# Performance work log

Hardware: AMD Instinct MI355X
Metric: run time of the kernel (lower is better)

Reference implementation:

```python
import jax, jax.numpy as jnp
import numpy as np

MAXDISP = 48
GROUP = 8
EPS = 1e-5


def setup_inputs() -> dict:
    key = jax.random.key(0)
    k1, k2 = jax.random.split(key)
    x = jax.random.normal(k1, (2, 64, 96, 320), dtype=jnp.float32)
    y = jax.random.normal(k2, (2, 64, 96, 320), dtype=jnp.float32)
    return {"x": x, "y": y}


def reference(x, y):
    # Faithful translation of CostVolume.forward.
    # torch's unfold over left-zero-padded y at kernel position d picks
    # y_pad[..., j + d]; per-window L2 norm over channels reduces to a
    # per-pixel channel norm (padded zeros normalize to zero), so we
    # normalize once and gather shifted columns.
    D = MAXDISP + 1
    b, c, h, w = x.shape
    cpg = c // GROUP
    xg = x.reshape(b, GROUP, cpg, h, w)
    yg = y.reshape(b, GROUP, cpg, h, w)
    xn = xg / (jnp.linalg.norm(xg, axis=2, keepdims=True) + EPS)
    yn = yg / (jnp.linalg.norm(yg, axis=2, keepdims=True) + EPS)
    # left zero-pad width dim by MAXDISP (padded zeros stay zero after norm)
    y_pad = jnp.pad(yn, ((0, 0), (0, 0), (0, 0), (0, 0), (MAXDISP, 0)))
    # after torch.flip on the disparity axis, disparity k compares x[:, j]
    # with y[:, j - k]  ->  padded index j + MAXDISP - k
    idx = jnp.arange(w)[None, :] + MAXDISP - jnp.arange(D)[:, None]  # [D, w]
    y_shift = y_pad[..., idx]  # [b, g, cpg, h, D, w]
    cost = jnp.sum(jnp.abs(xn[:, :, :, :, None, :] - y_shift), axis=2)  # [b,g,h,D,w]
    return jnp.transpose(cost, (0, 1, 3, 2, 4))  # [b, group, D, h, w]
```

## Files before the change

### kernel.cpp

```cpp
#include <hip/hip_runtime.h>


#define MAXDISP 48
#define NDISP   49
#define HH      96
#define WW      320
#define EPSN    1e-5f

__global__ __launch_bounds__(WW) void cost_volume_kernel(
    const float* __restrict__ x, const float* __restrict__ y,
    float* __restrict__ out)
{
    __shared__ float4 ylds[2 * WW];

    const int j   = threadIdx.x;
    const int blk = blockIdx.x;
    const int h   = blk % HH;
    const int bg  = blk / HH;

    const int inBase = bg * 8 * (HH * WW) + h * WW + j;

    float xv[8], yv[8];
    float xs = 0.f, ys = 0.f;
#pragma unroll
    for (int cc = 0; cc < 8; ++cc) {
        float xi = x[inBase + cc * (HH * WW)];
        float yi = y[inBase + cc * (HH * WW)];
        xv[cc] = xi; yv[cc] = yi;
        xs += xi * xi;
        ys += yi * yi;
    }
    const float xinv = 1.f / (sqrtf(xs) + EPSN);
    const float yinv = 1.f / (sqrtf(ys) + EPSN);

    float sAbs = 0.f;
#pragma unroll
    for (int cc = 0; cc < 8; ++cc) {
        xv[cc] *= xinv;
        yv[cc] *= yinv;
        sAbs += fabsf(xv[cc]);
    }

    ylds[j]      = make_float4(yv[0], yv[1], yv[2], yv[3]);
    ylds[WW + j] = make_float4(yv[4], yv[5], yv[6], yv[7]);
    __syncthreads();

    float* outp = out + bg * (NDISP * HH * WW) + h * WW + j;

#pragma unroll 7
    for (int d = 0; d < NDISP; ++d) {
        float cost;
        const int jj = j - d;
        if (jj >= 0) {
            const float4 a = ylds[jj];
            const float4 b = ylds[WW + jj];
            cost = fabsf(xv[0] - a.x) + fabsf(xv[1] - a.y)
                 + fabsf(xv[2] - a.z) + fabsf(xv[3] - a.w)
                 + fabsf(xv[4] - b.x) + fabsf(xv[5] - b.y)
                 + fabsf(xv[6] - b.z) + fabsf(xv[7] - b.w);
        } else {
            cost = sAbs;
        }
        outp[d * (HH * WW)] = cost;
    }
}

extern "C" void kernel_launch(void* const* d_in, const int* in_sizes, int n_in,
                              void* d_out, int out_size, void* d_ws, size_t ws_size,
                              hipStream_t stream) {
    const float* x = (const float*)d_in[0];
    const float* y = (const float*)d_in[1];
    float* out = (float*)d_out;
    dim3 grid(2 * 8 * HH);
    dim3 block(WW);
    cost_volume_kernel<<<grid, block, 0, stream>>>(x, y, out);
}
```

Baseline: 124.4 us.

## Register-tile cost volume over 4 pixels by 4 disparities with float4 stores

Each thread now computes a 4-pixel by 4-disparity tile instead of one pixel across all disparities. The 320 threads are split into 80 pixel quads and 4 disparity chunks. Normalized x and y are kept in LDS in channel-major layout, so y windows can be read with float4 loads and reused across disparities, and outputs are written as float4. This cuts LDS traffic per output and widens the global stores, at the cost of more registers and an uneven disparity split (the first chunk handles 4 groups, the others 3).

```diff
diff --git a/kernel.cpp b/kernel.cpp
--- a/kernel.cpp
+++ b/kernel.cpp
@@ -1,67 +1,108 @@
 #include <hip/hip_runtime.h>
 
 
-#define MAXDISP 48
-#define NDISP   49
-#define HH      96
-#define WW      320
-#define EPSN    1e-5f
+#define HH   96
+#define WW   320
+#define HW   (HH * WW)
+#define NDISP 49
+#define EPSN 1e-5f
 
 __global__ __launch_bounds__(WW) void cost_volume_kernel(
     const float* __restrict__ x, const float* __restrict__ y,
     float* __restrict__ out)
 {
-    __shared__ float4 ylds[2 * WW];
+    __shared__ float xn_s[8][WW];
+    __shared__ float yn_s[8][WW];
 
-    const int j   = threadIdx.x;
+    const int t   = threadIdx.x;
     const int blk = blockIdx.x;
     const int h   = blk % HH;
     const int bg  = blk / HH;
 
-    const int inBase = bg * 8 * (HH * WW) + h * WW + j;
+    const size_t inBase = (size_t)bg * 8 * HW + (size_t)h * WW;
 
-    float xv[8], yv[8];
-    float xs = 0.f, ys = 0.f;
+    {
+        float xv[8], yv[8];
+        float xs = 0.f, ys = 0.f;
+#pragma unroll
+        for (int cc = 0; cc < 8; ++cc) {
+            float xi = x[inBase + (size_t)cc * HW + t];
+            float yi = y[inBase + (size_t)cc * HW + t];
+            xv[cc] = xi; yv[cc] = yi;
+            xs += xi * xi;
+            ys += yi * yi;
+        }
+        const float xinv = 1.f / (sqrtf(xs) + EPSN);
+        const float yinv = 1.f / (sqrtf(ys) + EPSN);
+#pragma unroll
+        for (int cc = 0; cc < 8; ++cc) {
+            xn_s[cc][t] = xv[cc] * xinv;
+            yn_s[cc][t] = yv[cc] * yinv;
+        }
+    }
+    __syncthreads();
+
+    const int q  = t % 80;
+    const int dc = t / 80;
+    const int Q  = q * 4;
+
+    float4 xq[8];
+#pragma unroll
+    for (int cc = 0; cc < 8; ++cc)
+        xq[cc] = *(const float4*)&xn_s[cc][Q];
+
+    float4 sA = make_float4(0.f, 0.f, 0.f, 0.f);
 #pragma unroll
     for (int cc = 0; cc < 8; ++cc) {
-        float xi = x[inBase + cc * (HH * WW)];
-        float yi = y[inBase + cc * (HH * WW)];
-        xv[cc] = xi; yv[cc] = yi;
-        xs += xi * xi;
-        ys += yi * yi;
-    }
-    const float xinv = 1.f / (sqrtf(xs) + EPSN);
-    const float yinv = 1.f / (sqrtf(ys) + EPSN);
-
-    float sAbs = 0.f;
-#pragma unroll
-    for (int cc = 0; cc < 8; ++cc) {
-        xv[cc] *= xinv;
-        yv[cc] *= yinv;
-        sAbs += fabsf(xv[cc]);
+        sA.x += fabsf(xq[cc].x);
+        sA.y += fabsf(xq[cc].y);
+        sA.z += fabsf(xq[cc].z);
+        sA.w += fabsf(xq[cc].w);
     }
 
-    ylds[j]      = make_float4(yv[0], yv[1], yv[2], yv[3]);
-    ylds[WW + j] = make_float4(yv[4], yv[5], yv[6], yv[7]);
-    __syncthreads();
+    const int g0 = (dc == 0) ? 0 : (3 * dc + 1);
+    const int g1 = 3 * dc + 4;
 
-    float* outp = out + bg * (NDISP * HH * WW) + h * WW + j;
+    float* outp = out + (size_t)bg * (NDISP * HW) + (size_t)h * WW + Q;
 
-#pragma unroll 7
-    for (int d = 0; d < NDISP; ++d) {
-        float cost;
-        const int jj = j - d;
-        if (jj >= 0) {
-            const float4 a = ylds[jj];
-            const float4 b = ylds[WW + jj];
-            cost = fabsf(xv[0] - a.x) + fabsf(xv[1] - a.y)
-                 + fabsf(xv[2] - a.z) + fabsf(xv[3] - a.w)
-                 + fabsf(xv[4] - b.x) + fabsf(xv[5] - b.y)
-                 + fabsf(xv[6] - b.z) + fabsf(xv[7] - b.w);
-        } else {
-            cost = sAbs;
+    for (int g = g0; g < g1; ++g) {
+        int wq0 = q - g - 1; if (wq0 < 0) wq0 = 0;
+        int wq1 = q - g;     if (wq1 < 0) wq1 = 0;
+        const int a0 = wq0 * 4, a1 = wq1 * 4;
+
+        float acc[4][4];
+#pragma unroll
+        for (int e = 0; e < 4; ++e)
+#pragma unroll
+            for (int k = 0; k < 4; ++k) acc[e][k] = 0.f;
+
+#pragma unroll
+        for (int cc = 0; cc < 8; ++cc) {
+            const float4 wa = *(const float4*)&yn_s[cc][a0];
+            const float4 wb = *(const float4*)&yn_s[cc][a1];
+            const float win[8] = { wa.x, wa.y, wa.z, wa.w,
+                                   wb.x, wb.y, wb.z, wb.w };
+            const float4 xc = xq[cc];
+#pragma unroll
+            for (int e = 0; e < 4; ++e) {
+                acc[e][0] += fabsf(xc.x - win[4 - e]);
+                acc[e][1] += fabsf(xc.y - win[5 - e]);
+                acc[e][2] += fabsf(xc.z - win[6 - e]);
+                acc[e][3] += fabsf(xc.w - win[7 - e]);
+            }
         }
-        outp[d * (HH * WW)] = cost;
+
+#pragma unroll
+        for (int e = 0; e < 4; ++e) {
+            const int d = 4 * g + e;
+            float4 r;
+            r.x = (Q + 0 < d) ? sA.x : acc[e][0];
+            r.y = (Q + 1 < d) ? sA.y : acc[e][1];
+            r.z = (Q + 2 < d) ? sA.z : acc[e][2];
+            r.w = (Q + 3 < d) ? sA.w : acc[e][3];
+            if (d < NDISP)
+                *(float4*)&outp[(size_t)d * HW] = r;
+        }
     }
 }
 
```

Measured after the change: 138.0 us. 11.0% more time.
